# Kernel optimization log

Hardware: AMD Instinct MI355X
Metric: run time of the kernel (lower is better)

Reference implementation:

```python
import jax, jax.numpy as jnp
import numpy as np

H = 512  # hidden_dim


def setup_inputs() -> dict:
    key = jax.random.key(0)
    ks = jax.random.split(key, 9)
    B, T, TGT = 512, 512, 28
    s = 1.0 / np.sqrt(H)
    return {
        "sequence": jax.random.normal(ks[0], (B, T, 1), dtype=jnp.float32),
        "W_ih": jax.random.normal(ks[1], (4 * H, 1), dtype=jnp.float32) * s,
        "W_hh": jax.random.normal(ks[2], (4 * H, H), dtype=jnp.float32) * s,
        "b_ih": jax.random.normal(ks[3], (4 * H,), dtype=jnp.float32) * s,
        "b_hh": jax.random.normal(ks[4], (4 * H,), dtype=jnp.float32) * s,
        "fc1_w": jax.random.normal(ks[5], (H // 2, H), dtype=jnp.float32) * s,
        "fc1_b": jax.random.normal(ks[6], (H // 2,), dtype=jnp.float32) * s,
        "fc2_w": jax.random.normal(ks[7], (TGT, H // 2), dtype=jnp.float32) * (1.0 / np.sqrt(H // 2)),
        "fc2_b": jax.random.normal(ks[8], (TGT,), dtype=jnp.float32) * (1.0 / np.sqrt(H // 2)),
    }


def reference(sequence, W_ih, W_hh, b_ih, b_hh, fc1_w, fc1_b, fc2_w, fc2_b):
    B = sequence.shape[0]
    # Precompute input projections for all timesteps: [B,T,1] @ [1,4H] -> [T,B,4H]
    x_proj = jnp.einsum('bti,gi->tbg', sequence, W_ih) + b_ih + b_hh  # fold both biases

    def step(carry, xp):
        h, c = carry
        gates = xp + h @ W_hh.T                      # [B,4H]
        i, f, g, o = jnp.split(gates, 4, axis=-1)    # PyTorch LSTMCell gate order
        i = jax.nn.sigmoid(i)
        f = jax.nn.sigmoid(f)
        g = jnp.tanh(g)
        o = jax.nn.sigmoid(o)
        c_new = f * c + i * g
        h_new = o * jnp.tanh(c_new)
        return (h_new, c_new), None

    h0 = jnp.zeros((B, H), dtype=sequence.dtype)
    (h, _), _ = jax.lax.scan(step, (h0, h0), x_proj)

    # MLP head: Linear -> ReLU -> Linear, then unsqueeze to [B, target, 1]
    z = jax.nn.relu(h @ fc1_w.T + fc1_b)
    out = z @ fc2_w.T + fc2_b
    return out[:, :, None]
```

## Files before the change

### kernel.cpp

```cpp
#include <hip/hip_runtime.h>
#include <math.h>

#define H   512
#define B   512
#define T   512
#define TGT 28

typedef __bf16 bf16x8 __attribute__((ext_vector_type(8)));
typedef float  f32x4  __attribute__((ext_vector_type(4)));
typedef unsigned short u16;

#define OFF_WPH  0x000000u
#define OFF_WPL  0x200000u
#define OFF_HHI0 0x400000u
#define OFF_HLO0 0x480000u
#define OFF_SYNC 0x500000u
#define OFF_HHI1 0x501000u
#define OFF_HLO1 0x581000u

#define SMEM_BYTES 131072

__device__ inline u16 f2bf(float x) {
    unsigned u = __builtin_bit_cast(unsigned, x);
    u += 0x7FFFu + ((u >> 16) & 1u);
    return (u16)(u >> 16);
}
__device__ inline float bf2f(u16 h) {
    unsigned u = ((unsigned)h) << 16;
    return __builtin_bit_cast(float, u);
}
__device__ inline float frcp(float x) {
    float r = __builtin_amdgcn_rcpf(x);
    return r * fmaf(-x, r, 2.0f);
}
__device__ inline float fsig(float x) {
    return frcp(1.0f + __expf(-x));
}
__device__ inline float ftanh(float x) {
    return fmaf(2.0f, fsig(2.0f * x), -1.0f);
}

__global__ __launch_bounds__(256) void init_pack(const float* __restrict__ Whh,
                                                 u16* __restrict__ wph,
                                                 u16* __restrict__ wpl) {
    int idx = blockIdx.x * 256 + threadIdx.x;
    int l  = idx & 63;
    int S  = (idx >> 6) & 15;
    int q  = (idx >> 10) & 3;
    int r  = idx >> 12;
    int g  = q * 512 + r * 16 + (l & 15);
    int k  = S * 32 + ((l >> 4) * 8);
    const float* src = Whh + (size_t)g * H + k;
    __align__(16) u16 hi8[8];
    __align__(16) u16 lo8[8];
#pragma unroll
    for (int j = 0; j < 8; ++j) {
        float w = src[j];
        u16 hb = f2bf(w);
        hi8[j] = hb;
        lo8[j] = f2bf(w - bf2f(hb));
    }
    *(uint4*)(wph + (size_t)idx * 8) = *(const uint4*)hi8;
    *(uint4*)(wpl + (size_t)idx * 8) = *(const uint4*)lo8;
}

__global__ __launch_bounds__(256) void init_state(unsigned* __restrict__ zbase) {
    int idx = blockIdx.x * 256 + threadIdx.x;
    if (idx < 263168) zbase[idx] = 0u;
}

__global__ __launch_bounds__(512, 1) void lstm_persistent(
    const u16* __restrict__ wph, const u16* __restrict__ wpl,
    u16* __restrict__ hhi0, u16* __restrict__ hlo0,
    u16* __restrict__ hhi1, u16* __restrict__ hlo1,
    int* __restrict__ sync, const float* __restrict__ seq,
    const float* __restrict__ Wih, const float* __restrict__ bih,
    const float* __restrict__ bhh)
{
    extern __shared__ char smem[];
    u16* wh = (u16*)smem;
    u16* wl = wh + 32768;
    __shared__ __align__(16) float gatesT[64][68];

    const int tid  = threadIdx.x;
    const int l    = tid & 63;
    const int wave = tid >> 6;
    const int mt   = wave & 1;
    const int kh   = wave >> 1;

    __shared__ int sh_pr[2];
    if (tid == 0) {
        unsigned xcc;
        asm volatile("s_getreg_b32 %0, hwreg(HW_REG_XCC_ID)" : "=s"(xcc));
        int p = (int)(xcc & 7u);
        int r = __hip_atomic_fetch_add(&sync[p * 32], 1,
                                       __ATOMIC_RELAXED, __HIP_MEMORY_SCOPE_AGENT);
        sh_pr[0] = p;
        sh_pr[1] = r;
    }
    __syncthreads();
    const int p = sh_pr[0];
    const int r = sh_pr[1];
    int* arrp = &sync[256 + p * 32];

    {
        const uint4* gh = (const uint4*)(wph + (size_t)r * 32768);
        const uint4* gl = (const uint4*)(wpl + (size_t)r * 32768);
        uint4* sh = (uint4*)wh;
        uint4* sl = (uint4*)wl;
#pragma unroll
        for (int i = 0; i < 8; ++i) {
            int idx = tid + i * 512;
            sh[idx] = gh[idx];
            sl[idx] = gl[idx];
        }
    }

    const int cc   = tid & 15;
    const int m0   = tid >> 4;
    const int kcol = r * 16 + cc;
    float wib[4], bb[4];
#pragma unroll
    for (int q = 0; q < 4; ++q) {
        int g = q * 512 + kcol;
        wib[q] = Wih[g];
        bb[q]  = bih[g] + bhh[g];
    }
    float cr0 = 0.0f, cr1 = 0.0f;
    const int pb = p * 64;
    const int b0 = pb + m0;
    const int b1 = b0 + 32;

    const int arow0 = (pb + mt * 32 + (l & 15)) * H;
    const int arow1 = arow0 + 16 * H;

    __syncthreads();

    for (int t = 0; t < T; ++t) {
        const u16* hih = (t & 1) ? hhi1 : hhi0;
        const u16* hil = (t & 1) ? hlo1 : hlo0;
        u16* hoh = (t & 1) ? hhi0 : hhi1;
        u16* hol = (t & 1) ? hlo0 : hlo1;

        float sv0 = seq[(size_t)b0 * T + t];
        float sv1 = seq[(size_t)b1 * T + t];

        f32x4 acc[2][4] = {};

#pragma unroll 1
        for (int s = 0; s < 4; ++s) {
            const int S  = kh * 4 + s;
            const int ka = S * 32 + ((l >> 4) * 8);
            bf16x8 a0h = *(const bf16x8*)(hih + arow0 + ka);
            bf16x8 a1h = *(const bf16x8*)(hih + arow1 + ka);
            bf16x8 a0l = *(const bf16x8*)(hil + arow0 + ka);
            bf16x8 a1l = *(const bf16x8*)(hil + arow1 + ka);
#pragma unroll
            for (int n = 0; n < 4; ++n) {
                const int fo = ((n * 16 + S) * 64 + l) * 8;
                bf16x8 bh = *(const bf16x8*)(wh + fo);
                bf16x8 bl = *(const bf16x8*)(wl + fo);
                acc[0][n] = __builtin_amdgcn_mfma_f32_16x16x32_bf16(a0h, bh, acc[0][n], 0, 0, 0);
                acc[1][n] = __builtin_amdgcn_mfma_f32_16x16x32_bf16(a1h, bh, acc[1][n], 0, 0, 0);
                acc[0][n] = __builtin_amdgcn_mfma_f32_16x16x32_bf16(a0h, bl, acc[0][n], 0, 0, 0);
                acc[1][n] = __builtin_amdgcn_mfma_f32_16x16x32_bf16(a1h, bl, acc[1][n], 0, 0, 0);
                acc[0][n] = __builtin_amdgcn_mfma_f32_16x16x32_bf16(a0l, bh, acc[0][n], 0, 0, 0);
                acc[1][n] = __builtin_amdgcn_mfma_f32_16x16x32_bf16(a1l, bh, acc[1][n], 0, 0, 0);
            }
        }

#pragma unroll
        for (int rr = 0; rr < 4; ++rr) {
            if (kh == rr) {
#pragma unroll
                for (int ms = 0; ms < 2; ++ms)
#pragma unroll
                    for (int n = 0; n < 4; ++n) {
                        const int n2 = n * 16 + (l & 15);
                        const int mb = mt * 32 + ms * 16 + ((l >> 4) << 2);
                        float* gp = &gatesT[n2][mb];
                        if (rr == 0) {
                            *(f32x4*)gp = acc[ms][n];
                        } else {
                            f32x4 v = *(const f32x4*)gp;
                            v += acc[ms][n];
                            *(f32x4*)gp = v;
                        }
                    }
            }
            __syncthreads();
        }

        {
            float pre[4];
#pragma unroll
            for (int q = 0; q < 4; ++q) pre[q] = gatesT[q * 16 + cc][m0] + fmaf(sv0, wib[q], bb[q]);
            float ig = fsig(pre[0]);
            float fg = fsig(pre[1]);
            float gg = ftanh(pre[2]);
            float og = fsig(pre[3]);
            cr0 = fg * cr0 + ig * gg;
            float hv = og * ftanh(cr0);
            u16 hb = f2bf(hv);
            size_t ci = (size_t)b0 * H + kcol;
            hoh[ci] = hb;
            hol[ci] = f2bf(hv - bf2f(hb));
        }
        {
            float pre[4];
#pragma unroll
            for (int q = 0; q < 4; ++q) pre[q] = gatesT[q * 16 + cc][m0 + 32] + fmaf(sv1, wib[q], bb[q]);
            float ig = fsig(pre[0]);
            float fg = fsig(pre[1]);
            float gg = ftanh(pre[2]);
            float og = fsig(pre[3]);
            cr1 = fg * cr1 + ig * gg;
            float hv = og * ftanh(cr1);
            u16 hb = f2bf(hv);
            size_t ci = (size_t)b1 * H + kcol;
            hoh[ci] = hb;
            hol[ci] = f2bf(hv - bf2f(hb));
        }

        if (t < T - 1) {
            asm volatile("s_waitcnt vmcnt(0)" ::: "memory");
            __syncthreads();
            if (tid == 0) {
                __hip_atomic_fetch_add(arrp, 1, __ATOMIC_RELAXED,
                                       __HIP_MEMORY_SCOPE_WORKGROUP);
                const int target = 32 * (t + 1);
                int guard = 0;
                while (__hip_atomic_load(arrp, __ATOMIC_RELAXED,
                                         __HIP_MEMORY_SCOPE_AGENT) < target) {
                    __builtin_amdgcn_s_sleep(1);
                    if (++guard > (1 << 22)) break;
                }
            }
            __syncthreads();
            asm volatile("buffer_inv sc0" ::: "memory");
        }
    }
}

__global__ __launch_bounds__(256) void head_kernel(const u16* __restrict__ hhi,
                                                   const u16* __restrict__ hlo,
                                                   const float* __restrict__ fc1w,
                                                   const float* __restrict__ fc1b,
                                                   const float* __restrict__ fc2w,
                                                   const float* __restrict__ fc2b,
                                                   float* __restrict__ out) {
    const int b = blockIdx.x;
    const int tid = threadIdx.x;
    __shared__ __align__(16) float hb[H];
    __shared__ float z[256];

    hb[tid]       = bf2f(hhi[(size_t)b * H + tid])       + bf2f(hlo[(size_t)b * H + tid]);
    hb[tid + 256] = bf2f(hhi[(size_t)b * H + tid + 256]) + bf2f(hlo[(size_t)b * H + tid + 256]);
    __syncthreads();

    float acc = fc1b[tid];
    const float4* wr = (const float4*)(fc1w + (size_t)tid * H);
    const float4* hr = (const float4*)hb;
#pragma unroll 4
    for (int kk = 0; kk < H / 4; ++kk) {
        float4 wv = wr[kk], hv = hr[kk];
        acc += wv.x * hv.x + wv.y * hv.y + wv.z * hv.z + wv.w * hv.w;
    }
    z[tid] = fmaxf(acc, 0.0f);
    __syncthreads();

    if (tid < TGT) {
        float a = fc2b[tid];
        const float* w2 = fc2w + (size_t)tid * 256;
#pragma unroll 8
        for (int j = 0; j < 256; ++j) a += z[j] * w2[j];
        out[(size_t)b * TGT + tid] = a;
    }
}

extern "C" void kernel_launch(void* const* d_in, const int* in_sizes, int n_in,
                              void* d_out, int out_size, void* d_ws, size_t ws_size,
                              hipStream_t stream) {
    const float* seq  = (const float*)d_in[0];
    const float* Wih  = (const float*)d_in[1];
    const float* Whh  = (const float*)d_in[2];
    const float* bih  = (const float*)d_in[3];
    const float* bhh  = (const float*)d_in[4];
    const float* fc1w = (const float*)d_in[5];
    const float* fc1b = (const float*)d_in[6];
    const float* fc2w = (const float*)d_in[7];
    const float* fc2b = (const float*)d_in[8];
    float* out = (float*)d_out;

    char* wsb = (char*)d_ws;
    u16* wph  = (u16*)(wsb + OFF_WPH);
    u16* wpl  = (u16*)(wsb + OFF_WPL);
    u16* hhi0 = (u16*)(wsb + OFF_HHI0);
    u16* hlo0 = (u16*)(wsb + OFF_HLO0);
    u16* hhi1 = (u16*)(wsb + OFF_HHI1);
    u16* hlo1 = (u16*)(wsb + OFF_HLO1);
    int* sync = (int*)(wsb + OFF_SYNC);

    init_pack<<<512, 256, 0, stream>>>(Whh, wph, wpl);
    init_state<<<1028, 256, 0, stream>>>((unsigned*)(wsb + OFF_HHI0));

    hipFuncSetAttribute((const void*)lstm_persistent,
                        hipFuncAttributeMaxDynamicSharedMemorySize, SMEM_BYTES);

    void* args[] = {(void*)&wph, (void*)&wpl, (void*)&hhi0, (void*)&hlo0,
                    (void*)&hhi1, (void*)&hlo1, (void*)&sync, (void*)&seq,
                    (void*)&Wih, (void*)&bih, (void*)&bhh};
    hipLaunchCooperativeKernel((const void*)lstm_persistent, dim3(256), dim3(512),
                               args, SMEM_BYTES, stream);

    head_kernel<<<B, 256, 0, stream>>>(hhi0, hlo0, fc1w, fc1b, fc2w, fc2b, out);
}
```

Before: 4.818 ms.

## Split persistent LSTM block into two independent wave groups with LDS flag barriers

The 8 waves of each block are regrouped into two independent groups of 4 waves, each owning 32 batch rows, with their own gate scratch buffer. Block-wide __syncthreads calls are replaced by per-group LDS flag barriers, and each group keeps its own cross-block arrival counter at agent scope. The aim is to let the two halves of the block progress through time steps without waiting on each other and to shorten barrier latency. The cost is busy-wait spinning in LDS, which competes for issue slots and LDS bandwidth, and more fragile hand-written memory ordering.

```diff
diff --git a/kernel.cpp b/kernel.cpp
--- a/kernel.cpp
+++ b/kernel.cpp
@@ -38,6 +38,19 @@
 }
 __device__ inline float ftanh(float x) {
     return fmaf(2.0f, fsig(2.0f * x), -1.0f);
+}
+
+__device__ inline void group_barrier(int* gb, int kh, int l, int seq) {
+    if (l == 0)
+        __hip_atomic_store(&gb[kh], seq, __ATOMIC_RELEASE,
+                           __HIP_MEMORY_SCOPE_WORKGROUP);
+    int guard = 0;
+    for (;;) {
+        int v = __hip_atomic_load(&gb[l & 3], __ATOMIC_ACQUIRE,
+                                  __HIP_MEMORY_SCOPE_WORKGROUP);
+        if (__all(v >= seq)) break;
+        if (++guard > (1 << 17)) break;
+    }
 }
 
 __global__ __launch_bounds__(256) void init_pack(const float* __restrict__ Whh,
@@ -80,15 +93,17 @@
     extern __shared__ char smem[];
     u16* wh = (u16*)smem;
     u16* wl = wh + 32768;
-    __shared__ __align__(16) float gatesT[64][68];
-
-    const int tid  = threadIdx.x;
-    const int l    = tid & 63;
-    const int wave = tid >> 6;
-    const int mt   = wave & 1;
-    const int kh   = wave >> 1;
-
+    __shared__ __align__(16) float gatesT[2][64][36];
+    __shared__ int gbar[2][4];
+    __shared__ int grel[2];
     __shared__ int sh_pr[2];
+
+    const int tid = threadIdx.x;
+    const int l   = tid & 63;
+    const int w   = tid >> 6;
+    const int g   = w >> 2;
+    const int kh  = w & 3;
+
     if (tid == 0) {
         unsigned xcc;
         asm volatile("s_getreg_b32 %0, hwreg(HW_REG_XCC_ID)" : "=s"(xcc));
@@ -96,12 +111,15 @@
         int r = __hip_atomic_fetch_add(&sync[p * 32], 1,
                                        __ATOMIC_RELAXED, __HIP_MEMORY_SCOPE_AGENT);
         sh_pr[0] = p;
-        sh_pr[1] = r;
-    }
+        sh_pr[1] = r & 31;
+    }
+    if (tid < 8) gbar[tid >> 2][tid & 3] = 0;
+    if (tid < 2) grel[tid] = 0;
     __syncthreads();
     const int p = sh_pr[0];
     const int r = sh_pr[1];
-    int* arrp = &sync[256 + p * 32];
+    int* arrp = &sync[256 + p * 64 + g * 32];
+    int* gb   = gbar[g];
 
     {
         const uint4* gh = (const uint4*)(wph + (size_t)r * 32768);
@@ -116,22 +134,23 @@
         }
     }
 
-    const int cc   = tid & 15;
-    const int m0   = tid >> 4;
+    const int lt   = tid & 255;
+    const int cc   = lt & 15;
+    const int m0   = lt >> 4;
     const int kcol = r * 16 + cc;
     float wib[4], bb[4];
 #pragma unroll
     for (int q = 0; q < 4; ++q) {
-        int g = q * 512 + kcol;
-        wib[q] = Wih[g];
-        bb[q]  = bih[g] + bhh[g];
+        int gg = q * 512 + kcol;
+        wib[q] = Wih[gg];
+        bb[q]  = bih[gg] + bhh[gg];
     }
     float cr0 = 0.0f, cr1 = 0.0f;
     const int pb = p * 64;
-    const int b0 = pb + m0;
-    const int b1 = b0 + 32;
-
-    const int arow0 = (pb + mt * 32 + (l & 15)) * H;
+    const int b0 = pb + g * 32 + m0;
+    const int b1 = b0 + 16;
+
+    const int arow0 = (pb + g * 32 + (l & 15)) * H;
     const int arow1 = arow0 + 16 * H;
 
     __syncthreads();
@@ -169,6 +188,7 @@
             }
         }
 
+        const int base = t * 5;
 #pragma unroll
         for (int rr = 0; rr < 4; ++rr) {
             if (kh == rr) {
@@ -177,8 +197,8 @@
 #pragma unroll
                     for (int n = 0; n < 4; ++n) {
                         const int n2 = n * 16 + (l & 15);
-                        const int mb = mt * 32 + ms * 16 + ((l >> 4) << 2);
-                        float* gp = &gatesT[n2][mb];
+                        const int mb = ms * 16 + ((l >> 4) << 2);
+                        float* gp = &gatesT[g][n2][mb];
                         if (rr == 0) {
                             *(f32x4*)gp = acc[ms][n];
                         } else {
@@ -188,18 +208,18 @@
                         }
                     }
             }
-            __syncthreads();
+            group_barrier(gb, kh, l, base + rr + 1);
         }
 
         {
             float pre[4];
 #pragma unroll
-            for (int q = 0; q < 4; ++q) pre[q] = gatesT[q * 16 + cc][m0] + fmaf(sv0, wib[q], bb[q]);
+            for (int q = 0; q < 4; ++q) pre[q] = gatesT[g][q * 16 + cc][m0] + fmaf(sv0, wib[q], bb[q]);
             float ig = fsig(pre[0]);
             float fg = fsig(pre[1]);
-            float gg = ftanh(pre[2]);
+            float gg2 = ftanh(pre[2]);
             float og = fsig(pre[3]);
-            cr0 = fg * cr0 + ig * gg;
+            cr0 = fg * cr0 + ig * gg2;
             float hv = og * ftanh(cr0);
             u16 hb = f2bf(hv);
             size_t ci = (size_t)b0 * H + kcol;
@@ -209,12 +229,12 @@
         {
             float pre[4];
 #pragma unroll
-            for (int q = 0; q < 4; ++q) pre[q] = gatesT[q * 16 + cc][m0 + 32] + fmaf(sv1, wib[q], bb[q]);
+            for (int q = 0; q < 4; ++q) pre[q] = gatesT[g][q * 16 + cc][m0 + 16] + fmaf(sv1, wib[q], bb[q]);
             float ig = fsig(pre[0]);
             float fg = fsig(pre[1]);
-            float gg = ftanh(pre[2]);
+            float gg2 = ftanh(pre[2]);
             float og = fsig(pre[3]);
-            cr1 = fg * cr1 + ig * gg;
+            cr1 = fg * cr1 + ig * gg2;
             float hv = og * ftanh(cr1);
             u16 hb = f2bf(hv);
             size_t ci = (size_t)b1 * H + kcol;
@@ -224,19 +244,27 @@
 
         if (t < T - 1) {
             asm volatile("s_waitcnt vmcnt(0)" ::: "memory");
-            __syncthreads();
-            if (tid == 0) {
+            group_barrier(gb, kh, l, base + 5);
+            if (kh == 0 && l == 0) {
                 __hip_atomic_fetch_add(arrp, 1, __ATOMIC_RELAXED,
-                                       __HIP_MEMORY_SCOPE_WORKGROUP);
+                                       __HIP_MEMORY_SCOPE_AGENT);
                 const int target = 32 * (t + 1);
                 int guard = 0;
                 while (__hip_atomic_load(arrp, __ATOMIC_RELAXED,
                                          __HIP_MEMORY_SCOPE_AGENT) < target) {
                     __builtin_amdgcn_s_sleep(1);
-                    if (++guard > (1 << 22)) break;
+                    if (++guard > (1 << 18)) break;
+                }
+                __hip_atomic_store(&grel[g], t + 1, __ATOMIC_RELEASE,
+                                   __HIP_MEMORY_SCOPE_WORKGROUP);
+            }
+            {
+                int guard = 0;
+                while (__hip_atomic_load(&grel[g], __ATOMIC_ACQUIRE,
+                                         __HIP_MEMORY_SCOPE_WORKGROUP) < t + 1) {
+                    if (++guard > (1 << 17)) break;
                 }
             }
-            __syncthreads();
             asm volatile("buffer_inv sc0" ::: "memory");
         }
     }
```

Result: faster. 4.181 ms (-13.2%).
